# Kernel tuning notes

Hardware: AMD Instinct MI355X
Metric: run time of the kernel (lower is better)

Reference implementation:

```python
import jax, jax.numpy as jnp
import numpy as np

N = 100000
E = 1600000
F_IN = 256
H1, C1 = 8, 8          # conv1: 8 heads x 8 channels -> 64
H2, C2 = 1, 32         # conv2: 1 head x num_classes
SLOPE = 0.2


def gat_conv(x, src, dst, n, W, a_src, a_dst, b, heads, out):
    # x: [n, f_in]; W: [f_in, heads*out]; a_src/a_dst: [heads, out]; b: [heads*out]
    h = (x @ W).reshape(n, heads, out)                       # [n, H, C]
    s = jnp.sum(h * a_src, axis=-1)                          # [n, H]
    d = jnp.sum(h * a_dst, axis=-1)                          # [n, H]
    e = jax.nn.leaky_relu(s[src] + d[dst], SLOPE)            # [e, H]
    m = jax.ops.segment_max(e, dst, num_segments=n)          # stable segment softmax
    ex = jnp.exp(e - m[dst])
    z = jax.ops.segment_sum(ex, dst, num_segments=n)
    alpha = ex / (z[dst] + 1e-16)                            # [e, H]
    msg = alpha[:, :, None] * h[src]                         # [e, H, C]
    agg = jax.ops.segment_sum(msg, dst, num_segments=n)      # [n, H, C]
    return agg.reshape(n, heads * out) + b


def setup_inputs() -> dict:
    key = jax.random.key(0)
    ks = jax.random.split(key, 10)
    x = jax.random.normal(ks[0], (N, F_IN), dtype=jnp.float32)
    edge_index = jax.random.randint(ks[1], (2, E), 0, N, dtype=jnp.int32)
    sc = 0.05
    W1 = jax.random.normal(ks[2], (F_IN, H1 * C1), dtype=jnp.float32) * sc
    att_src1 = jax.random.normal(ks[3], (H1, C1), dtype=jnp.float32) * sc
    att_dst1 = jax.random.normal(ks[4], (H1, C1), dtype=jnp.float32) * sc
    b1 = jnp.zeros((H1 * C1,), dtype=jnp.float32)
    W2 = jax.random.normal(ks[5], (H1 * C1, H2 * C2), dtype=jnp.float32) * sc
    att_src2 = jax.random.normal(ks[6], (H2, C2), dtype=jnp.float32) * sc
    att_dst2 = jax.random.normal(ks[7], (H2, C2), dtype=jnp.float32) * sc
    b2 = jnp.zeros((H2 * C2,), dtype=jnp.float32)
    return {"x": x, "edge_index": edge_index, "W1": W1, "att_src1": att_src1,
            "att_dst1": att_dst1, "b1": b1, "W2": W2, "att_src2": att_src2,
            "att_dst2": att_dst2, "b2": b2}


def reference(x, edge_index, W1, att_src1, att_dst1, b1, W2, att_src2, att_dst2, b2):
    # add self loops (PyG GATConv default)
    loops = jnp.arange(N, dtype=edge_index.dtype)
    src = jnp.concatenate([edge_index[0], loops])
    dst = jnp.concatenate([edge_index[1], loops])
    # dropout layers are identity in eval mode
    h = gat_conv(x, src, dst, N, W1, att_src1, att_dst1, b1, H1, C1)
    h = jax.nn.elu(h)
    h = gat_conv(h, src, dst, N, W2, att_src2, att_dst2, b2, H2, C2)
    return jax.nn.log_softmax(h, axis=1)
```

## Files before the change

### kernel.cpp

```cpp
#include <hip/hip_runtime.h>
#include <hip/hip_bf16.h>

#define N_NODES 100000
#define N_EDGES 1600000
#define N_TOT   (N_EDGES + N_NODES)
#define F_IN    256
#define F1      64
#define H1      8
#define C1      8
#define F2      32
#define SLOPE   0.2f

#define NB_G    ((N_NODES + 255) / 256)

#define EB      4096
#define NB1     ((N_EDGES + EB - 1) / EB)
#define BW      256
#define NBKT    ((N_NODES + BW - 1) / BW)

typedef unsigned int  uint;
typedef unsigned short ushort;
typedef __attribute__((ext_vector_type(8))) short bf16x8;
typedef __attribute__((ext_vector_type(4))) float f32x4;
typedef __attribute__((ext_vector_type(2))) float f32x2;

__device__ inline ushort f2bf(float f) {
    uint u = __float_as_uint(f);
    uint r = u + 0x7fffu + ((u >> 16) & 1u);
    return (ushort)(r >> 16);
}
__device__ inline float bflo(uint u) { return __uint_as_float(u << 16); }
__device__ inline float bfhi(uint u) { return __uint_as_float(u & 0xffff0000u); }
__device__ inline uint pk2bf(float a, float b) {
    __hip_bfloat162 h = __float22bfloat162_rn(make_float2(a, b));
    union { __hip_bfloat162 h; uint u; } cv; cv.h = h;
    return cv.u;
}

__device__ inline void bucket_bases(const int* __restrict__ colsum,
                                    int* sc, int* sb, int tid) {
    const int i0 = 2 * tid, i1 = 2 * tid + 1;
    const int a0 = (i0 < NBKT) ? colsum[i0] : 0;
    const int a1 = (i1 < NBKT) ? colsum[i1] : 0;
    sc[tid] = a0 + a1;
    __syncthreads();
    for (int off = 1; off < 256; off <<= 1) {
        int t = (tid >= off) ? sc[tid - off] : 0;
        __syncthreads();
        sc[tid] += t;
        __syncthreads();
    }
    const int excl = sc[tid] - (a0 + a1);
    if (i0 < NBKT)  sb[i0] = excl;
    if (i1 <= NBKT) sb[i1] = excl + a0;
    __syncthreads();
}

__global__ __launch_bounds__(256) void k_p1w(
        const int* __restrict__ ei, const float* __restrict__ W1,
        int* __restrict__ bcnt, ushort* __restrict__ w1b) {
    __shared__ int H[NBKT];
    const int tid = threadIdx.x;
    if (blockIdx.x == NB1) {
        for (int i = 0; i < 64; ++i) {
            const int e = i * 256 + tid;
            const int k = e >> 6, n = e & 63;
            w1b[((k >> 3) * 64 + n) * 8 + (k & 7)] = f2bf(W1[e]);
        }
        return;
    }
    const int blk = blockIdx.x;
    for (int j = tid; j < NBKT; j += 256) H[j] = 0;
    __syncthreads();
    const int e0 = blk * EB;
    const int lim = (e0 + EB < N_EDGES) ? e0 + EB : N_EDGES;
    for (int i = e0 + tid; i < lim; i += 256)
        atomicAdd(&H[ei[N_EDGES + i] >> 8], 1);
    __syncthreads();
    for (int j = tid; j < NBKT; j += 256)
        bcnt[j * NB1 + blk] = H[j];
}

__global__ __launch_bounds__(64) void k_p2(
        int* __restrict__ bcnt, int* __restrict__ colsum) {
    const int col = blockIdx.x, lane = threadIdx.x;
    int carry = 0;
    for (int c0 = 0; c0 < NB1; c0 += 64) {
        const int idx = c0 + lane;
        const int v = (idx < NB1) ? bcnt[col * NB1 + idx] : 0;
        int s = v;
#pragma unroll
        for (int off = 1; off < 64; off <<= 1) {
            int u = __shfl_up(s, off);
            if (lane >= off) s += u;
        }
        if (idx < NB1) bcnt[col * NB1 + idx] = carry + s - v;
        carry += __shfl(s, 63);
    }
    if (lane == 0) colsum[col] = carry;
}

__global__ __launch_bounds__(256) void k_p3(
        const int* __restrict__ ei, const int* __restrict__ bcnt,
        const int* __restrict__ colsum, uint* __restrict__ tmp) {
    __shared__ int sc[256];
    __shared__ int cur[NBKT + 1];
    const int tid = threadIdx.x, blk = blockIdx.x;
    bucket_bases(colsum, sc, cur, tid);
    for (int b = tid; b < NBKT; b += 256) cur[b] += bcnt[b * NB1 + blk];
    __syncthreads();
    const int e0 = blk * EB;
    const int lim = (e0 + EB < N_EDGES) ? e0 + EB : N_EDGES;
    for (int i = e0 + tid; i < lim; i += 256) {
        const int s = ei[i], d = ei[N_EDGES + i];
        const int pos = atomicAdd(&cur[d >> 8], 1);
        tmp[pos] = ((uint)(d & 255) << 24) | (uint)s;
    }
}

__global__ __launch_bounds__(256) void k_final_gemm(
        const uint* __restrict__ tmp, const int* __restrict__ colsum,
        int* __restrict__ row_ptr, int* __restrict__ srcs,
        const float* __restrict__ x, const ushort* __restrict__ w1b,
        const float* __restrict__ as1, const float* __restrict__ ad1,
        ushort* __restrict__ h1b, float* __restrict__ s1,
        float* __restrict__ d1) {
    __shared__ union {
        struct { int sc[256]; int sb[NBKT + 1]; int cur[BW]; } f;
        ushort B[F_IN * F1];
        ushort S[4][64][66];
    } sm;
    const int tid = threadIdx.x;

    if (blockIdx.x < NBKT) {
        const int b = blockIdx.x;
        bucket_bases(colsum, sm.f.sc, sm.f.sb, tid);
        sm.f.cur[tid] = 0;
        __syncthreads();
        const int lo = sm.f.sb[b], hi = sm.f.sb[b + 1];
        for (int i = lo + tid; i < hi; i += 256)
            atomicAdd(&sm.f.cur[tmp[i] >> 24], 1);
        __syncthreads();
        const int n = b * BW + tid;
        const int myc = sm.f.cur[tid];
        const int v = (n < N_NODES) ? myc + 1 : 0;
        __syncthreads();
        sm.f.sc[tid] = v;
        __syncthreads();
        for (int off = 1; off < 256; off <<= 1) {
            int t = (tid >= off) ? sm.f.sc[tid - off] : 0;
            __syncthreads();
            sm.f.sc[tid] += t;
            __syncthreads();
        }
        const int rp = lo + b * BW + (sm.f.sc[tid] - v);
        if (n < N_NODES) {
            row_ptr[n] = rp;
            srcs[rp] = n;
        }
        if (b == NBKT - 1 && tid == 255) row_ptr[N_NODES] = N_TOT;
        sm.f.cur[tid] = rp + 1;
        __syncthreads();
        for (int i = lo + tid; i < hi; i += 256) {
            const uint u = tmp[i];
            const int pos = atomicAdd(&sm.f.cur[u >> 24], 1);
            srcs[pos] = (int)(u & 0xFFFFFFu);
        }
        return;
    }

    {
        const uint4* s4 = (const uint4*)w1b;
        uint4* d4 = (uint4*)sm.B;
#pragma unroll
        for (int i = 0; i < 8; ++i)
            d4[i * 256 + tid] = s4[i * 256 + tid];
    }
    __syncthreads();

    const int wave = tid >> 6, lane = tid & 63;
    const int q = lane >> 4, ln = lane & 15;
    const int rowbase = (blockIdx.x - NBKT) * 256 + wave * 64;

    f32x4 acc[4][4];
#pragma unroll
    for (int mt = 0; mt < 4; ++mt)
#pragma unroll
        for (int nt = 0; nt < 4; ++nt) acc[mt][nt] = (f32x4){0.f, 0.f, 0.f, 0.f};

    int rows[4];
#pragma unroll
    for (int mt = 0; mt < 4; ++mt) {
        const int r = rowbase + mt * 16 + ln;
        rows[mt] = r < N_NODES ? r : N_NODES - 1;
    }

    for (int t = 0; t < 8; ++t) {
        bf16x8 bfr[4];
#pragma unroll
        for (int nt = 0; nt < 4; ++nt)
            bfr[nt] = *(const bf16x8*)&sm.B[((t * 4 + q) * 64 + nt * 16 + ln) * 8];
#pragma unroll
        for (int mt = 0; mt < 4; ++mt) {
            const float4* ap = (const float4*)(x + (size_t)rows[mt] * F_IN + t * 32 + q * 8);
            const float4 a0 = ap[0], a1 = ap[1];
            uint4 au = make_uint4(pk2bf(a0.x, a0.y), pk2bf(a0.z, a0.w),
                                  pk2bf(a1.x, a1.y), pk2bf(a1.z, a1.w));
            bf16x8 af = *(bf16x8*)&au;
#pragma unroll
            for (int nt = 0; nt < 4; ++nt)
                acc[mt][nt] = __builtin_amdgcn_mfma_f32_16x16x32_bf16(
                                  af, bfr[nt], acc[mt][nt], 0, 0, 0);
        }
    }
    __syncthreads();

#pragma unroll
    for (int mt = 0; mt < 4; ++mt)
#pragma unroll
        for (int nt = 0; nt < 4; ++nt)
#pragma unroll
            for (int r = 0; r < 4; ++r)
                sm.S[wave][mt * 16 + q * 4 + r][nt * 16 + ln] = f2bf(acc[mt][nt][r]);
    __syncthreads();

    const int node = rowbase + lane;
    if (node >= N_NODES) return;
    const uint* srow = (const uint*)&sm.S[wave][lane][0];
    float sacc[H1], dacc[H1];
#pragma unroll
    for (int h = 0; h < H1; ++h) { sacc[h] = 0.f; dacc[h] = 0.f; }
    uint4* hout = (uint4*)(h1b + (size_t)node * F1);
#pragma unroll
    for (int p4 = 0; p4 < 8; ++p4) {
        const uint u0 = srow[p4 * 4 + 0], u1 = srow[p4 * 4 + 1];
        const uint u2 = srow[p4 * 4 + 2], u3 = srow[p4 * 4 + 3];
        hout[p4] = make_uint4(u0, u1, u2, u3);
        const float c[8] = {bflo(u0), bfhi(u0), bflo(u1), bfhi(u1),
                            bflo(u2), bfhi(u2), bflo(u3), bfhi(u3)};
#pragma unroll
        for (int j = 0; j < 8; ++j) {
            sacc[p4] += c[j] * as1[p4 * 8 + j];
            dacc[p4] += c[j] * ad1[p4 * 8 + j];
        }
    }
    float4* s4 = (float4*)(s1 + (size_t)node * H1);
    float4* d4 = (float4*)(d1 + (size_t)node * H1);
    s4[0] = make_float4(sacc[0], sacc[1], sacc[2], sacc[3]);
    s4[1] = make_float4(sacc[4], sacc[5], sacc[6], sacc[7]);
    d4[0] = make_float4(dacc[0], dacc[1], dacc[2], dacc[3]);
    d4[1] = make_float4(dacc[4], dacc[5], dacc[6], dacc[7]);
}

__global__ __launch_bounds__(256) void k_agg1(
        const int* __restrict__ row_ptr, const int* __restrict__ srcs,
        const ushort* __restrict__ h1b, const float* __restrict__ s1,
        const float* __restrict__ d1, const float* __restrict__ b1,
        const float* __restrict__ W2, const float* __restrict__ as2,
        const float* __restrict__ ad2,
        ushort* __restrict__ h2b, float* __restrict__ s2,
        float* __restrict__ d2) {
    __shared__ float sx[4][64];
    const int wid = (blockIdx.x * 256 + threadIdx.x) >> 6;
    if (wid >= N_NODES) return;
    const int w = threadIdx.x >> 6;
    const int lane = threadIdx.x & 63;
    const int q = lane >> 3;
    const int c = lane & 7;
    const float dh = d1[(size_t)wid * H1 + c];
    const int beg = row_ptr[wid], end = row_ptr[wid + 1];
    const uint4* hv = (const uint4*)h1b;
    f32x2 A0 = {0.f, 0.f}, A1 = {0.f, 0.f}, A2 = {0.f, 0.f}, A3 = {0.f, 0.f};
    float z = 0.f;
    int i = beg + q;
    for (; i + 8 < end; i += 16) {
        const int sA = srcs[i], sB = srcs[i + 8];
        float eA = s1[(size_t)sA * H1 + c] + dh;
        float eB = s1[(size_t)sB * H1 + c] + dh;
        eA = fmaxf(eA, SLOPE * eA);
        eB = fmaxf(eB, SLOPE * eB);
        const float xA = __expf(eA), xB = __expf(eB);
        const uint4 UA = hv[(size_t)sA * 8 + c];
        const uint4 UB = hv[(size_t)sB * 8 + c];
        z += xA + xB;
        const f32x2 xa = {xA, xA}, xb = {xB, xB};
        A0 += xa * (f32x2){bflo(UA.x), bfhi(UA.x)};
        A1 += xa * (f32x2){bflo(UA.y), bfhi(UA.y)};
        A2 += xa * (f32x2){bflo(UA.z), bfhi(UA.z)};
        A3 += xa * (f32x2){bflo(UA.w), bfhi(UA.w)};
        A0 += xb * (f32x2){bflo(UB.x), bfhi(UB.x)};
        A1 += xb * (f32x2){bflo(UB.y), bfhi(UB.y)};
        A2 += xb * (f32x2){bflo(UB.z), bfhi(UB.z)};
        A3 += xb * (f32x2){bflo(UB.w), bfhi(UB.w)};
    }
    for (; i < end; i += 8) {
        const int sA = srcs[i];
        float eA = s1[(size_t)sA * H1 + c] + dh;
        eA = fmaxf(eA, SLOPE * eA);
        const float xA = __expf(eA);
        const uint4 UA = hv[(size_t)sA * 8 + c];
        z += xA;
        const f32x2 xa = {xA, xA};
        A0 += xa * (f32x2){bflo(UA.x), bfhi(UA.x)};
        A1 += xa * (f32x2){bflo(UA.y), bfhi(UA.y)};
        A2 += xa * (f32x2){bflo(UA.z), bfhi(UA.z)};
        A3 += xa * (f32x2){bflo(UA.w), bfhi(UA.w)};
    }
    f32x2 r0, r1;
    {
        const bool hi = lane & 8;
        f32x2 snd0 = hi ? A0 : A2, snd1 = hi ? A1 : A3;
        const f32x2 kp0 = hi ? A2 : A0, kp1 = hi ? A3 : A1;
        snd0.x = __shfl_xor(snd0.x, 8); snd0.y = __shfl_xor(snd0.y, 8);
        snd1.x = __shfl_xor(snd1.x, 8); snd1.y = __shfl_xor(snd1.y, 8);
        r0 = kp0 + snd0; r1 = kp1 + snd1;
    }
    {
        const bool hi = lane & 16;
        f32x2 snd = hi ? r0 : r1;
        const f32x2 kp = hi ? r1 : r0;
        snd.x = __shfl_xor(snd.x, 16); snd.y = __shfl_xor(snd.y, 16);
        r0 = kp + snd;
    }
    float sv;
    {
        const bool hi = lane & 32;
        float snd = hi ? r0.x : r0.y;
        const float kp = hi ? r0.y : r0.x;
        snd = __shfl_xor(snd, 32);
        sv = kp + snd;
    }
    z += __shfl_xor(z, 8); z += __shfl_xor(z, 16); z += __shfl_xor(z, 32);

    const int j = (((lane >> 3) & 1) << 2) | (((lane >> 4) & 1) << 1)
                | ((lane >> 5) & 1);
    const int xi = c * 8 + j;
    const float zi = 1.f / (z + 1e-16f);
    float xv = sv * zi + b1[xi];
    xv = xv > 0.f ? xv : __expf(xv) - 1.f;
    sx[w][xi] = xv;
    __builtin_amdgcn_wave_barrier();

    const int kh = lane >> 5;
    const int oc = lane & 31;
    const float4* sxv = (const float4*)&sx[w][kh * 32];
    const float* wp0 = W2 + (size_t)(kh * 32) * F2 + oc;
    float acc = 0.f;
#pragma unroll
    for (int k4 = 0; k4 < 8; ++k4) {
        const float4 xv4 = sxv[k4];
        const float* wp = wp0 + (size_t)k4 * 4 * F2;
        acc += xv4.x * wp[0]      + xv4.y * wp[F2]
             + xv4.z * wp[2 * F2] + xv4.w * wp[3 * F2];
    }
    acc += __shfl_xor(acc, 32);

    float sA2 = acc * as2[oc], dA2 = acc * ad2[oc];
#pragma unroll
    for (int off = 1; off <= 16; off <<= 1) {
        sA2 += __shfl_xor(sA2, off);
        dA2 += __shfl_xor(dA2, off);
    }
    const float accp = __shfl_xor(acc, 1);
    if (lane < 32 && !(lane & 1))
        *(uint*)&h2b[(size_t)wid * F2 + oc] = pk2bf(acc, accp);
    if (lane == 0) { s2[wid] = sA2; d2[wid] = dA2; }
}

__global__ __launch_bounds__(256) void k_agg2(
        const int* __restrict__ row_ptr, const int* __restrict__ srcs,
        const ushort* __restrict__ h2b, const float* __restrict__ s2,
        const float* __restrict__ d2, const float* __restrict__ b2,
        float* __restrict__ out) {
    const int wid = (blockIdx.x * 256 + threadIdx.x) >> 6;
    if (wid >= N_NODES) return;
    const int lane = threadIdx.x & 63;
    const int q = lane >> 2;
    const int c = lane & 3;
    const float dn = d2[wid];
    const int beg = row_ptr[wid], end = row_ptr[wid + 1];
    const uint4* hv = (const uint4*)h2b;
    f32x2 A0 = {0.f, 0.f}, A1 = {0.f, 0.f}, A2 = {0.f, 0.f}, A3 = {0.f, 0.f};
    float z = 0.f;
    int i = beg + q;
    for (; i + 16 < end; i += 32) {
        const int sA = srcs[i], sB = srcs[i + 16];
        float eA = s2[sA] + dn;
        float eB = s2[sB] + dn;
        eA = fmaxf(eA, SLOPE * eA);
        eB = fmaxf(eB, SLOPE * eB);
        const float xA = __expf(eA), xB = __expf(eB);
        const uint4 UA = hv[(size_t)sA * 4 + c];
        const uint4 UB = hv[(size_t)sB * 4 + c];
        z += xA + xB;
        const f32x2 xa = {xA, xA}, xb = {xB, xB};
        A0 += xa * (f32x2){bflo(UA.x), bfhi(UA.x)};
        A1 += xa * (f32x2){bflo(UA.y), bfhi(UA.y)};
        A2 += xa * (f32x2){bflo(UA.z), bfhi(UA.z)};
        A3 += xa * (f32x2){bflo(UA.w), bfhi(UA.w)};
        A0 += xb * (f32x2){bflo(UB.x), bfhi(UB.x)};
        A1 += xb * (f32x2){bflo(UB.y), bfhi(UB.y)};
        A2 += xb * (f32x2){bflo(UB.z), bfhi(UB.z)};
        A3 += xb * (f32x2){bflo(UB.w), bfhi(UB.w)};
    }
    for (; i < end; i += 16) {
        const int sA = srcs[i];
        float eA = s2[sA] + dn;
        eA = fmaxf(eA, SLOPE * eA);
        const float xA = __expf(eA);
        const uint4 UA = hv[(size_t)sA * 4 + c];
        z += xA;
        const f32x2 xa = {xA, xA};
        A0 += xa * (f32x2){bflo(UA.x), bfhi(UA.x)};
        A1 += xa * (f32x2){bflo(UA.y), bfhi(UA.y)};
        A2 += xa * (f32x2){bflo(UA.z), bfhi(UA.z)};
        A3 += xa * (f32x2){bflo(UA.w), bfhi(UA.w)};
    }
    f32x2 r0, r1;
    {
        const bool hi = lane & 4;
        f32x2 snd0 = hi ? A0 : A2, snd1 = hi ? A1 : A3;
        const f32x2 kp0 = hi ? A2 : A0, kp1 = hi ? A3 : A1;
        snd0.x = __shfl_xor(snd0.x, 4); snd0.y = __shfl_xor(snd0.y, 4);
        snd1.x = __shfl_xor(snd1.x, 4); snd1.y = __shfl_xor(snd1.y, 4);
        r0 = kp0 + snd0; r1 = kp1 + snd1;
    }
    {
        const bool hi = lane & 8;
        f32x2 snd = hi ? r0 : r1;
        const f32x2 kp = hi ? r1 : r0;
        snd.x = __shfl_xor(snd.x, 8); snd.y = __shfl_xor(snd.y, 8);
        r0 = kp + snd;
    }
    float sv;
    {
        const bool hi = lane & 16;
        float snd = hi ? r0.x : r0.y;
        const float kp = hi ? r0.y : r0.x;
        snd = __shfl_xor(snd, 16);
        sv = kp + snd;
    }
    sv += __shfl_xor(sv, 32);
    z += __shfl_xor(z, 4); z += __shfl_xor(z, 8);
    z += __shfl_xor(z, 16); z += __shfl_xor(z, 32);

    const int j = (((lane >> 2) & 1) << 2) | (((lane >> 3) & 1) << 1)
                | ((lane >> 4) & 1);
    const int elem = c * 8 + j;
    const float zi = 1.f / (z + 1e-16f);
    const float v = sv * zi + b2[elem];
    float m = v;
#pragma unroll
    for (int off = 1; off <= 16; off <<= 1) m = fmaxf(m, __shfl_xor(m, off));
    float ssum = __expf(v - m);
#pragma unroll
    for (int off = 1; off <= 16; off <<= 1) ssum += __shfl_xor(ssum, off);
    const float lse = m + __logf(ssum);
    if (lane < 32) out[(size_t)wid * F2 + elem] = v - lse;
}

extern "C" void kernel_launch(void* const* d_in, const int* in_sizes, int n_in,
                              void* d_out, int out_size, void* d_ws, size_t ws_size,
                              hipStream_t stream) {
    const float* x   = (const float*)d_in[0];
    const int*   ei  = (const int*)d_in[1];
    const float* W1  = (const float*)d_in[2];
    const float* as1 = (const float*)d_in[3];
    const float* ad1 = (const float*)d_in[4];
    const float* b1  = (const float*)d_in[5];
    const float* W2  = (const float*)d_in[6];
    const float* as2 = (const float*)d_in[7];
    const float* ad2 = (const float*)d_in[8];
    const float* b2  = (const float*)d_in[9];
    float* out = (float*)d_out;

    ushort* h1b = (ushort*)d_ws;
    ushort* h2b = h1b + (size_t)N_NODES * F1;
    ushort* w1b = h2b + (size_t)N_NODES * F2;
    float*  s1  = (float*)(w1b + F_IN * F1);
    float*  d1  = s1 + (size_t)N_NODES * H1;
    float*  s2  = d1 + (size_t)N_NODES * H1;
    float*  d2  = s2 + N_NODES;
    uint*   tmp = (uint*)(d2 + N_NODES);
    int* row_ptr = (int*)(tmp + N_EDGES);
    int* colsum  = row_ptr + N_NODES + 1;
    int* bcnt    = colsum + NBKT;
    int* srcs    = bcnt + (size_t)NBKT * NB1;

    const int nb_w = (N_NODES * 64 + 255) / 256;

    k_p1w<<<NB1 + 1, 256, 0, stream>>>(ei, W1, bcnt, w1b);
    k_p2<<<NBKT, 64, 0, stream>>>(bcnt, colsum);
    k_p3<<<NB1, 256, 0, stream>>>(ei, bcnt, colsum, tmp);
    k_final_gemm<<<NBKT + NB_G, 256, 0, stream>>>(tmp, colsum, row_ptr, srcs,
                                                  x, w1b, as1, ad1,
                                                  h1b, s1, d1);
    k_agg1<<<nb_w, 256, 0, stream>>>(row_ptr, srcs, h1b, s1, d1, b1,
                                     W2, as2, ad2, h2b, s2, d2);
    k_agg2<<<nb_w, 256, 0, stream>>>(row_ptr, srcs, h2b, s2, d2, b2, out);
}
```

Before: 354.3 us.

## Pre-convert x to bf16 in the histogram kernel and feed GEMM bf16 rows

Adds 3125 blocks to the first kernel that convert the fp32 input features to bf16 in a workspace buffer, overlapping with the edge histogram work. The GEMM then loads bf16 rows directly and batches its A-fragment loads ahead of the MFMAs, with partial unrolling. This takes the per-element conversion out of the GEMM inner loop. In exchange it writes and rereads an extra 51 MB bf16 copy of x, so total memory traffic goes up.

```diff
diff --git a/kernel.cpp b/kernel.cpp
--- a/kernel.cpp
+++ b/kernel.cpp
@@ -12,6 +12,7 @@
 #define SLOPE   0.2f
 
 #define NB_G    ((N_NODES + 255) / 256)
+#define NB_X    3125
 
 #define EB      4096
 #define NB1     ((N_EDGES + EB - 1) / EB)
@@ -58,10 +59,22 @@
 
 __global__ __launch_bounds__(256) void k_p1w(
         const int* __restrict__ ei, const float* __restrict__ W1,
-        int* __restrict__ bcnt, ushort* __restrict__ w1b) {
+        const float* __restrict__ x,
+        int* __restrict__ bcnt, ushort* __restrict__ w1b,
+        ushort* __restrict__ xb) {
     __shared__ int H[NBKT];
     const int tid = threadIdx.x;
-    if (blockIdx.x == NB1) {
+    if (blockIdx.x < NB_X) {
+        const size_t base = (size_t)blockIdx.x * 8192;
+#pragma unroll
+        for (int r = 0; r < 8; ++r) {
+            const size_t idx = base + (size_t)r * 1024 + tid * 4;
+            const float4 v = *(const float4*)(x + idx);
+            *(uint2*)(xb + idx) = make_uint2(pk2bf(v.x, v.y), pk2bf(v.z, v.w));
+        }
+        return;
+    }
+    if (blockIdx.x == NB_X) {
         for (int i = 0; i < 64; ++i) {
             const int e = i * 256 + tid;
             const int k = e >> 6, n = e & 63;
@@ -69,7 +82,7 @@
         }
         return;
     }
-    const int blk = blockIdx.x;
+    const int blk = blockIdx.x - NB_X - 1;
     for (int j = tid; j < NBKT; j += 256) H[j] = 0;
     __syncthreads();
     const int e0 = blk * EB;
@@ -121,7 +134,7 @@
 __global__ __launch_bounds__(256) void k_final_gemm(
         const uint* __restrict__ tmp, const int* __restrict__ colsum,
         int* __restrict__ row_ptr, int* __restrict__ srcs,
-        const float* __restrict__ x, const ushort* __restrict__ w1b,
+        const ushort* __restrict__ xb, const ushort* __restrict__ w1b,
         const float* __restrict__ as1, const float* __restrict__ ad1,
         ushort* __restrict__ h1b, float* __restrict__ s1,
         float* __restrict__ d1) {
@@ -188,30 +201,30 @@
 #pragma unroll
         for (int nt = 0; nt < 4; ++nt) acc[mt][nt] = (f32x4){0.f, 0.f, 0.f, 0.f};
 
-    int rows[4];
+    const ushort* xrow[4];
 #pragma unroll
     for (int mt = 0; mt < 4; ++mt) {
         const int r = rowbase + mt * 16 + ln;
-        rows[mt] = r < N_NODES ? r : N_NODES - 1;
-    }
-
+        const int rc = r < N_NODES ? r : N_NODES - 1;
+        xrow[mt] = xb + (size_t)rc * F_IN + q * 8;
+    }
+
+#pragma unroll 4
     for (int t = 0; t < 8; ++t) {
         bf16x8 bfr[4];
 #pragma unroll
         for (int nt = 0; nt < 4; ++nt)
             bfr[nt] = *(const bf16x8*)&sm.B[((t * 4 + q) * 64 + nt * 16 + ln) * 8];
-#pragma unroll
-        for (int mt = 0; mt < 4; ++mt) {
-            const float4* ap = (const float4*)(x + (size_t)rows[mt] * F_IN + t * 32 + q * 8);
-            const float4 a0 = ap[0], a1 = ap[1];
-            uint4 au = make_uint4(pk2bf(a0.x, a0.y), pk2bf(a0.z, a0.w),
-                                  pk2bf(a1.x, a1.y), pk2bf(a1.z, a1.w));
-            bf16x8 af = *(bf16x8*)&au;
+        bf16x8 af[4];
+#pragma unroll
+        for (int mt = 0; mt < 4; ++mt)
+            af[mt] = *(const bf16x8*)(xrow[mt] + t * 32);
+#pragma unroll
+        for (int mt = 0; mt < 4; ++mt)
 #pragma unroll
             for (int nt = 0; nt < 4; ++nt)
                 acc[mt][nt] = __builtin_amdgcn_mfma_f32_16x16x32_bf16(
-                                  af, bfr[nt], acc[mt][nt], 0, 0, 0);
-        }
+                                  af[mt], bfr[nt], acc[mt][nt], 0, 0, 0);
     }
     __syncthreads();
 
@@ -283,15 +296,15 @@
         const uint4 UA = hv[(size_t)sA * 8 + c];
         const uint4 UB = hv[(size_t)sB * 8 + c];
         z += xA + xB;
-        const f32x2 xa = {xA, xA}, xb = {xB, xB};
+        const f32x2 xa = {xA, xA}, xb2 = {xB, xB};
         A0 += xa * (f32x2){bflo(UA.x), bfhi(UA.x)};
         A1 += xa * (f32x2){bflo(UA.y), bfhi(UA.y)};
         A2 += xa * (f32x2){bflo(UA.z), bfhi(UA.z)};
         A3 += xa * (f32x2){bflo(UA.w), bfhi(UA.w)};
-        A0 += xb * (f32x2){bflo(UB.x), bfhi(UB.x)};
-        A1 += xb * (f32x2){bflo(UB.y), bfhi(UB.y)};
-        A2 += xb * (f32x2){bflo(UB.z), bfhi(UB.z)};
-        A3 += xb * (f32x2){bflo(UB.w), bfhi(UB.w)};
+        A0 += xb2 * (f32x2){bflo(UB.x), bfhi(UB.x)};
+        A1 += xb2 * (f32x2){bflo(UB.y), bfhi(UB.y)};
+        A2 += xb2 * (f32x2){bflo(UB.z), bfhi(UB.z)};
+        A3 += xb2 * (f32x2){bflo(UB.w), bfhi(UB.w)};
     }
     for (; i < end; i += 8) {
         const int sA = srcs[i];
@@ -393,15 +406,15 @@
         const uint4 UA = hv[(size_t)sA * 4 + c];
         const uint4 UB = hv[(size_t)sB * 4 + c];
         z += xA + xB;
-        const f32x2 xa = {xA, xA}, xb = {xB, xB};
+        const f32x2 xa = {xA, xA}, xb2 = {xB, xB};
         A0 += xa * (f32x2){bflo(UA.x), bfhi(UA.x)};
         A1 += xa * (f32x2){bflo(UA.y), bfhi(UA.y)};
         A2 += xa * (f32x2){bflo(UA.z), bfhi(UA.z)};
         A3 += xa * (f32x2){bflo(UA.w), bfhi(UA.w)};
-        A0 += xb * (f32x2){bflo(UB.x), bfhi(UB.x)};
-        A1 += xb * (f32x2){bflo(UB.y), bfhi(UB.y)};
-        A2 += xb * (f32x2){bflo(UB.z), bfhi(UB.z)};
-        A3 += xb * (f32x2){bflo(UB.w), bfhi(UB.w)};
+        A0 += xb2 * (f32x2){bflo(UB.x), bfhi(UB.x)};
+        A1 += xb2 * (f32x2){bflo(UB.y), bfhi(UB.y)};
+        A2 += xb2 * (f32x2){bflo(UB.z), bfhi(UB.z)};
+        A3 += xb2 * (f32x2){bflo(UB.w), bfhi(UB.w)};
     }
     for (; i < end; i += 16) {
         const int sA = srcs[i];
@@ -474,7 +487,8 @@
     const float* b2  = (const float*)d_in[9];
     float* out = (float*)d_out;
 
-    ushort* h1b = (ushort*)d_ws;
+    ushort* xb  = (ushort*)d_ws;
+    ushort* h1b = xb + (size_t)N_NODES * F_IN;
     ushort* h2b = h1b + (size_t)N_NODES * F1;
     ushort* w1b = h2b + (size_t)N_NODES * F2;
     float*  s1  = (float*)(w1b + F_IN * F1);
@@ -489,11 +503,11 @@
 
     const int nb_w = (N_NODES * 64 + 255) / 256;
 
-    k_p1w<<<NB1 + 1, 256, 0, stream>>>(ei, W1, bcnt, w1b);
+    k_p1w<<<NB_X + 1 + NB1, 256, 0, stream>>>(ei, W1, x, bcnt, w1b, xb);
     k_p2<<<NBKT, 64, 0, stream>>>(bcnt, colsum);
     k_p3<<<NB1, 256, 0, stream>>>(ei, bcnt, colsum, tmp);
     k_final_gemm<<<NBKT + NB_G, 256, 0, stream>>>(tmp, colsum, row_ptr, srcs,
-                                                  x, w1b, as1, ad1,
+                                                  xb, w1b, as1, ad1,
                                                   h1b, s1, d1);
     k_agg1<<<nb_w, 256, 0, stream>>>(row_ptr, srcs, h1b, s1, d1, b1,
                                      W2, as2, ad2, h2b, s2, d2);
```

Result: no change. 347.6 us (-1.9%).
